# Kernel tuning notes

Measured on AMD Instinct MI355X. Metric: run time of the kernel, lower is better.

Reference implementation:

```python
import jax, jax.numpy as jnp
from jax import lax
import numpy as np

B, T, FEAT = 32, 256, 640
H, P = 2048, 640  # lstm_hidden_units, lstm_projection
FORGET_BIAS = 1.0  # TF v1 LSTMCell default


def setup_inputs() -> dict:
    key = jax.random.key(0)
    ks = jax.random.split(key, 6)
    s = 0.02  # small init so tanh/sigmoid stay well-conditioned
    return {
        "x": jax.random.normal(ks[0], (B, T, FEAT), dtype=jnp.float32),
        "W0": jax.random.normal(ks[1], (FEAT + P, 4 * H), dtype=jnp.float32) * s,
        "b0": jnp.zeros((4 * H,), dtype=jnp.float32),
        "P0": jax.random.normal(ks[2], (H, P), dtype=jnp.float32) * s,
        "W1": jax.random.normal(ks[3], (P + P, 4 * H), dtype=jnp.float32) * s,
        "b1": jnp.zeros((4 * H,), dtype=jnp.float32),
        "P1": jax.random.normal(ks[4], (H, P), dtype=jnp.float32) * s,
    }


def _lstmp_layer(x, W, b, proj):
    # x: [B, T, D]; TF v1 LSTMCell with num_proj, gate order (i, j, f, o)
    batch = x.shape[0]
    c0 = jnp.zeros((batch, H), dtype=x.dtype)
    m0 = jnp.zeros((batch, proj.shape[1]), dtype=x.dtype)

    def step(carry, xt):
        c, m = carry
        z = jnp.concatenate([xt, m], axis=-1) @ W + b  # [B, 4H]
        i, j, f, o = jnp.split(z, 4, axis=-1)
        c_new = jax.nn.sigmoid(f + FORGET_BIAS) * c + jax.nn.sigmoid(i) * jnp.tanh(j)
        m_new = (jax.nn.sigmoid(o) * jnp.tanh(c_new)) @ proj  # [B, P]
        return (c_new, m_new), m_new

    xT = jnp.swapaxes(x, 0, 1)  # [T, B, D]
    _, ys = lax.scan(step, (c0, m0), xT)
    return jnp.swapaxes(ys, 0, 1)  # [B, T, P]


def reference(x, W0, b0, P0, W1, b1, P1):
    h = _lstmp_layer(x, W0, b0, P0)
    h = _lstmp_layer(h, W1, b1, P1)
    return h
```

## Files before the change

### kernel.cpp

```cpp
#include <hip/hip_runtime.h>
#include <math.h>

typedef __attribute__((ext_vector_type(8))) short s16x8;
typedef __attribute__((ext_vector_type(8))) _Float16 f16x8;
typedef __attribute__((ext_vector_type(16))) float f32x16;
typedef unsigned long long u64;
typedef unsigned short u16;

#define NBLK 256
#define NTHR 512

constexpr int HSZ2 = 32 * 2048;

__device__ __forceinline__ float sigm(float v) { return 1.0f / (1.0f + expf(-v)); }

__device__ __forceinline__ unsigned short bf16_rne(float x) {
    unsigned u = __float_as_uint(x);
    return (unsigned short)((u + 0x7FFFu + ((u >> 16) & 1u)) >> 16);
}
__device__ __forceinline__ void split2(float x, unsigned short& hi, unsigned short& lo) {
    unsigned u = __float_as_uint(x);
    hi = (unsigned short)(u >> 16);
    float hf = __uint_as_float(u & 0xFFFF0000u);
    lo = bf16_rne(x - hf);
}
__device__ __forceinline__ void split8(const float* f, s16x8& h, s16x8& l) {
    #pragma unroll
    for (int i = 0; i < 8; ++i) {
        unsigned short hh, ll;
        split2(f[i], hh, ll);
        h[i] = (short)hh; l[i] = (short)ll;
    }
}

__device__ __forceinline__ void ast64(u16* p, u64 v) {
    __hip_atomic_store((u64*)p, v, __ATOMIC_RELAXED, __HIP_MEMORY_SCOPE_AGENT);
}

__device__ __forceinline__ void pollall(const unsigned* arr, unsigned e) {
    if (threadIdx.x < 64) {
        const int i0 = (int)threadIdx.x * 4;
        for (;;) {
            bool ok = (__hip_atomic_load(arr + i0 + 0, __ATOMIC_RELAXED, __HIP_MEMORY_SCOPE_AGENT) >= e) &&
                      (__hip_atomic_load(arr + i0 + 1, __ATOMIC_RELAXED, __HIP_MEMORY_SCOPE_AGENT) >= e) &&
                      (__hip_atomic_load(arr + i0 + 2, __ATOMIC_RELAXED, __HIP_MEMORY_SCOPE_AGENT) >= e) &&
                      (__hip_atomic_load(arr + i0 + 3, __ATOMIC_RELAXED, __HIP_MEMORY_SCOPE_AGENT) >= e);
            if (__all(ok)) break;
            __builtin_amdgcn_s_sleep(1);
        }
    }
    __syncthreads();
}

__global__ void transpose_split(const float* __restrict__ in,
                                u16* __restrict__ outHi, u16* __restrict__ outLo,
                                int R, int C) {
    __shared__ float tile[32][33];
    const int c0 = blockIdx.x * 32, r0 = blockIdx.y * 32;
    const int tid = threadIdx.x;
    {
        int r = tid >> 3, q = (tid & 7) * 4;
        float4 v = *(const float4*)(in + (size_t)(r0 + r) * C + c0 + q);
        tile[q + 0][r] = v.x; tile[q + 1][r] = v.y;
        tile[q + 2][r] = v.z; tile[q + 3][r] = v.w;
    }
    __syncthreads();
    {
        int c = tid >> 3, q = (tid & 7) * 4;
        ushort4 h, l;
        unsigned short hh, ll;
        split2(tile[c][q + 0], hh, ll); h.x = hh; l.x = ll;
        split2(tile[c][q + 1], hh, ll); h.y = hh; l.y = ll;
        split2(tile[c][q + 2], hh, ll); h.z = hh; l.z = ll;
        split2(tile[c][q + 3], hh, ll); h.w = hh; l.w = ll;
        size_t o = (size_t)(c0 + c) * R + r0 + q;
        *(ushort4*)(outHi + o) = h;
        *(ushort4*)(outLo + o) = l;
    }
}

__global__ void transpose_f16(const float* __restrict__ in, u16* __restrict__ outp,
                              int R, int C) {
    __shared__ float tile[32][33];
    const int c0 = blockIdx.x * 32, r0 = blockIdx.y * 32;
    const int tid = threadIdx.x;
    {
        int r = tid >> 3, q = (tid & 7) * 4;
        float4 v = *(const float4*)(in + (size_t)(r0 + r) * C + c0 + q);
        tile[q + 0][r] = v.x; tile[q + 1][r] = v.y;
        tile[q + 2][r] = v.z; tile[q + 3][r] = v.w;
    }
    __syncthreads();
    {
        int c = tid >> 3, q = (tid & 7) * 4;
        ushort4 o;
        o.x = __builtin_bit_cast(u16, (_Float16)tile[c][q + 0]);
        o.y = __builtin_bit_cast(u16, (_Float16)tile[c][q + 1]);
        o.z = __builtin_bit_cast(u16, (_Float16)tile[c][q + 2]);
        o.w = __builtin_bit_cast(u16, (_Float16)tile[c][q + 3]);
        *(ushort4*)(outp + (size_t)(c0 + c) * R + r0 + q) = o;
    }
}

__global__ void xcast(const float* __restrict__ in, u16* __restrict__ outp, int n4) {
    int i = blockIdx.x * blockDim.x + threadIdx.x;
    if (i < n4) {
        float4 v = ((const float4*)in)[i];
        ushort4 o;
        o.x = __builtin_bit_cast(u16, (_Float16)v.x);
        o.y = __builtin_bit_cast(u16, (_Float16)v.y);
        o.z = __builtin_bit_cast(u16, (_Float16)v.z);
        o.w = __builtin_bit_cast(u16, (_Float16)v.w);
        ((ushort4*)outp)[i] = o;
    }
}

__global__ void __launch_bounds__(256) qgemm(const float* __restrict__ P,
    const u16* __restrict__ WH, const u16* __restrict__ WL,
    u16* __restrict__ Qt, int rowOff) {
    const int tid = threadIdx.x;
    const int wid = tid >> 6, lane = tid & 63;
    const int n = lane & 31, kg = lane >> 5;
    const int tile = blockIdx.x * 4 + wid;
    const int ct = tile & 255, kt = tile >> 8;
    const int col = ct * 32 + n;
    const int krow = kt * 32 + n;

    f32x16 acc;
    #pragma unroll
    for (int r = 0; r < 16; ++r) acc[r] = 0.f;

    const float* ap = P + (size_t)krow * 640 + kg * 8;
    const u16* bhp = WH + (size_t)col * 1280 + rowOff + kg * 8;
    const u16* blp = WL + (size_t)col * 1280 + rowOff + kg * 8;
    #pragma unroll 4
    for (int ks = 0; ks < 40; ++ks) {
        float4 v0 = *(const float4*)(ap + ks * 16);
        float4 v1 = *(const float4*)(ap + ks * 16 + 4);
        float f[8] = {v0.x, v0.y, v0.z, v0.w, v1.x, v1.y, v1.z, v1.w};
        s16x8 ah, al;
        split8(f, ah, al);
        s16x8 bh = *(const s16x8*)(bhp + ks * 16);
        s16x8 bl = *(const s16x8*)(blp + ks * 16);
        acc = __builtin_amdgcn_mfma_f32_32x32x16_bf16(ah, bh, acc, 0, 0, 0);
        acc = __builtin_amdgcn_mfma_f32_32x32x16_bf16(ah, bl, acc, 0, 0, 0);
        acc = __builtin_amdgcn_mfma_f32_32x32x16_bf16(al, bh, acc, 0, 0, 0);
    }
    u16* qrow = Qt + (size_t)col * 2048 + kt * 32 + 4 * kg;
    #pragma unroll
    for (int q = 0; q < 4; ++q) {
        ushort4 o;
        o.x = __builtin_bit_cast(u16, (_Float16)acc[4 * q + 0]);
        o.y = __builtin_bit_cast(u16, (_Float16)acc[4 * q + 1]);
        o.z = __builtin_bit_cast(u16, (_Float16)acc[4 * q + 2]);
        o.w = __builtin_bit_cast(u16, (_Float16)acc[4 * q + 3]);
        *(ushort4*)(qrow + 8 * q) = o;
    }
}

__global__ void __launch_bounds__(NTHR, 1) lstm_pipe(
    const u16* __restrict__ xh,
    const float* __restrict__ bias0, const float* __restrict__ bias1,
    const u16* __restrict__ Wxt0,
    const u16* __restrict__ Qt0, const u16* __restrict__ Qt01, const u16* __restrict__ Qt1,
    const u16* __restrict__ Pt1,
    u16* __restrict__ hb0, u16* __restrict__ hb1,
    float* out, unsigned* arr) {
    __shared__ float part0[8][64][20];
    __shared__ float part1[8][64][20];
    __shared__ u16 hst0[32][8];
    __shared__ u16 hst1[32][8];

    const int tid = threadIdx.x, bid = blockIdx.x;
    const int wid = tid >> 6, lane = tid & 63;
    const int n = lane & 31, kg = lane >> 5;

    const int colmap = (n >> 3) * 2048 + bid * 8 + (n & 7);
    const size_t wx640 = (size_t)colmap * 640 + wid * 80 + kg * 8;
    const size_t qOff  = (size_t)colmap * 2048 + wid * 256 + kg * 8;
    const size_t aXh   = (size_t)n * (256 * 640) + wid * 80 + kg * 8;
    const size_t hROff = (size_t)n * 2048 + wid * 256 + kg * 8;

    const int rn = tid >> 4, rm0 = (tid & 15) * 2;

    const bool isC0 = tid < 256;
    const int cl = tid & 255;
    const int ch = cl >> 5, cb = cl & 31;
    float bv[4];
    #pragma unroll
    for (int gx = 0; gx < 4; ++gx)
        bv[gx] = (isC0 ? bias0 : bias1)[gx * 2048 + bid * 8 + ch];
    const int crg = (cb & 3) + 4 * (cb >> 3);
    const int clp = 32 * ((cb >> 2) & 1);

    uint4 q0r[16], q01r[16], q1r[16];
    #pragma unroll
    for (int ks = 0; ks < 16; ++ks) {
        q0r[ks]  = *(const uint4*)(Qt0  + qOff + ks * 16);
        q01r[ks] = *(const uint4*)(Qt01 + qOff + ks * 16);
        q1r[ks]  = *(const uint4*)(Qt1  + qOff + ks * 16);
    }
    #pragma unroll
    for (int ks = 0; ks < 16; ++ks) {
        asm volatile("" : "+v"(q0r[ks].x),  "+v"(q0r[ks].y),  "+v"(q0r[ks].z),  "+v"(q0r[ks].w));
        asm volatile("" : "+v"(q01r[ks].x), "+v"(q01r[ks].y), "+v"(q01r[ks].z), "+v"(q01r[ks].w));
        asm volatile("" : "+v"(q1r[ks].x),  "+v"(q1r[ks].y),  "+v"(q1r[ks].z),  "+v"(q1r[ks].w));
    }

    float creg = 0.f;

    auto xp0 = [&](int t) -> f32x16 {
        f32x16 a;
        #pragma unroll
        for (int r = 0; r < 16; ++r) a[r] = 0.f;
        const u16* xb = xh + aXh + (size_t)t * 640;
        const u16* wb = Wxt0 + wx640;
        #pragma unroll
        for (int ks = 0; ks < 5; ++ks)
            a = __builtin_amdgcn_mfma_f32_32x32x16_f16(*(const f16x8*)(xb + ks * 16),
                                                       *(const f16x8*)(wb + ks * 16), a, 0, 0, 0);
        return a;
    };
    auto stash = [&](float (*prt)[64][20], const f32x16& v) {
        #pragma unroll
        for (int r = 0; r < 4; ++r) {
            float4 w;
            w.x = v[4 * r + 0]; w.y = v[4 * r + 1];
            w.z = v[4 * r + 2]; w.w = v[4 * r + 3];
            *(float4*)&prt[wid][lane][4 * r] = w;
        }
    };

    f32x16 zacc0 = xp0(0);

    for (int g = 0; g <= 256; ++g) {
        if (g > 0) pollall(arr, (unsigned)g);
        const int s = g - 1;
        const bool doL0 = (g <= 255);
        const bool doL1 = (s >= 0);

        f32x16 acc0, acc1;
        if (doL0) acc0 = zacc0;
        if (doL1) {
            #pragma unroll
            for (int r = 0; r < 16; ++r) acc1[r] = 0.f;
        }
        if (g >= 1) {
            const u16* h0c = hb0 + (size_t)(g - 1) * HSZ2 + hROff;
            if (doL0) {
                #pragma unroll
                for (int ks = 0; ks < 16; ++ks) {
                    f16x8 a = *(const f16x8*)(h0c + ks * 16);
                    acc0 = __builtin_amdgcn_mfma_f32_32x32x16_f16(a, __builtin_bit_cast(f16x8, q0r[ks]),  acc0, 0, 0, 0);
                    acc1 = __builtin_amdgcn_mfma_f32_32x32x16_f16(a, __builtin_bit_cast(f16x8, q01r[ks]), acc1, 0, 0, 0);
                }
            } else {
                #pragma unroll
                for (int ks = 0; ks < 16; ++ks)
                    acc1 = __builtin_amdgcn_mfma_f32_32x32x16_f16(*(const f16x8*)(h0c + ks * 16),
                                                                  __builtin_bit_cast(f16x8, q01r[ks]), acc1, 0, 0, 0);
            }
        }
        if (s >= 1) {
            const u16* h1c = hb1 + (size_t)(s - 1) * HSZ2 + hROff;
            #pragma unroll
            for (int ks = 0; ks < 16; ++ks)
                acc1 = __builtin_amdgcn_mfma_f32_32x32x16_f16(*(const f16x8*)(h1c + ks * 16),
                                                              __builtin_bit_cast(f16x8, q1r[ks]), acc1, 0, 0, 0);
        }

        if (doL0) stash(part0, acc0);
        if (doL1) stash(part1, acc1);
        __syncthreads();
        if ((isC0 && doL0) || (!isC0 && doL1)) {
            float (*prt)[64][20] = isC0 ? part0 : part1;
            float z[4];
            #pragma unroll
            for (int gx = 0; gx < 4; ++gx) {
                const int lp = (gx * 8 + ch) + clp;
                float ssum = 0.f;
                #pragma unroll
                for (int w = 0; w < 8; ++w) ssum += prt[w][lp][crg];
                z[gx] = ssum + bv[gx];
            }
            float cn = sigm(z[2] + 1.0f) * creg + sigm(z[0]) * tanhf(z[1]);
            creg = cn;
            u16 hv = __builtin_bit_cast(u16, (_Float16)(sigm(z[3]) * tanhf(cn)));
            if (isC0) hst0[cb][ch] = hv;
            else      hst1[cb][ch] = hv;
        }
        __syncthreads();

        if (doL0 && wid == 0) {
            int b = tid >> 1, hf = tid & 1;
            u64 v = *(const u64*)&hst0[b][hf * 4];
            ast64(hb0 + (size_t)g * HSZ2 + (size_t)b * 2048 + bid * 8 + hf * 4, v);
        }
        if (doL1 && wid == 1) {
            int l = tid - 64;
            int b = l >> 1, hf = l & 1;
            u64 v = *(const u64*)&hst1[b][hf * 4];
            ast64(hb1 + (size_t)s * HSZ2 + (size_t)b * 2048 + bid * 8 + hf * 4, v);
        }
        __syncthreads();
        if (tid == 0)
            __hip_atomic_store(arr + bid, (unsigned)(g + 1), __ATOMIC_RELAXED, __HIP_MEMORY_SCOPE_AGENT);

        if (g < 255) zacc0 = xp0(g + 1);
    }

    pollall(arr, 257u);
    const int mb = bid >> 3;
    const int t0 = (bid * 32) & 255;
    const size_t aOff = (size_t)(t0 + n) * HSZ2 + (size_t)mb * 2048 + wid * 256 + kg * 8;
    for (int ct = 0; ct < 20; ++ct) {
        f32x16 pacc;
        #pragma unroll
        for (int r = 0; r < 16; ++r) pacc[r] = 0.f;
        const u16* ap = hb1 + aOff;
        const u16* bp = Pt1 + (size_t)(ct * 32 + n) * 2048 + wid * 256 + kg * 8;
        #pragma unroll
        for (int ks = 0; ks < 16; ++ks)
            pacc = __builtin_amdgcn_mfma_f32_32x32x16_f16(*(const f16x8*)(ap + ks * 16),
                                                          *(const f16x8*)(bp + ks * 16), pacc, 0, 0, 0);
        __syncthreads();
        stash(part0, pacc);
        __syncthreads();
        #pragma unroll
        for (int j = 0; j < 2; ++j) {
            int m = rm0 + j;
            int lp = rn + 32 * ((m >> 2) & 1);
            int rg = (m & 3) + 4 * (m >> 3);
            float ssum = 0.f;
            #pragma unroll
            for (int w = 0; w < 8; ++w) ssum += part0[w][lp][rg];
            out[(size_t)(bid * 32 + m) * 640 + ct * 32 + rn] = ssum;
        }
    }
}

__device__ __forceinline__ void grid_bar_slow(unsigned int* bar, unsigned int& epoch) {
    __syncthreads();
    epoch++;
    if (threadIdx.x == 0) {
        __threadfence();
        atomicAdd(bar, 1u);
        const unsigned int target = epoch * NBLK;
        while (__hip_atomic_load(bar, __ATOMIC_RELAXED, __HIP_MEMORY_SCOPE_AGENT) < target)
            __builtin_amdgcn_s_sleep(1);
        __threadfence();
    }
    __syncthreads();
}

__global__ void __launch_bounds__(NTHR, 1) lstm_fb(
    const float* __restrict__ x,
    const float* __restrict__ W0, const float* __restrict__ b0, const float* __restrict__ Pr0,
    const float* __restrict__ W1, const float* __restrict__ b1, const float* __restrict__ Pr1,
    float* out, float* ws) {
    const int tid = threadIdx.x;
    const int bid = blockIdx.x;
    unsigned int* bar = (unsigned int*)ws;
    float* mbuf0 = ws + 1024;
    float* mbuf1 = mbuf0 + 32 * 640;
    float* hws = mbuf1 + 32 * 640;
    __shared__ float zbuf[32 * 33];
    __shared__ float pred[512];
    unsigned int epoch = 0;
    const int c_idx = tid & 31;
    const int bg = tid >> 5;
    const int b0r = bg * 2;
    const int col = (c_idx >> 3) * 2048 + bid * 8 + (c_idx & 7);
    const int ch = tid >> 5;
    const int cb = tid & 31;
    const int p_s = (bid * 640) / NBLK;
    const int p_e = ((bid + 1) * 640) / NBLK;
    const int np = p_e - p_s;
    const int kq_n = (np == 2) ? 8 : 4;
    const int klen = 2048 / kq_n;
    const int pg = tid >> 5;
    const bool pact = pg < np * kq_n;
    const int pj = pact ? (pg % np) : 0;
    const int kq = pact ? (pg / np) : 0;
    for (int layer = 0; layer < 2; ++layer) {
        const float* W = layer ? W1 : W0;
        const float* bbv = layer ? b1 : b0;
        const float* Pr = layer ? Pr1 : Pr0;
        const float* inb = layer ? (const float*)out : x;
        for (int i = bid * NTHR + tid; i < 32 * 640; i += NBLK * NTHR) mbuf0[i] = 0.0f;
        float creg = 0.0f;
        grid_bar_slow(bar, epoch);
        const float bias = bbv[col];
        for (int t = 0; t < 256; ++t) {
            float* mcur = (t & 1) ? mbuf1 : mbuf0;
            float* mnxt = (t & 1) ? mbuf0 : mbuf1;
            const float* in0 = inb + (size_t)(b0r * 256 + t) * 640;
            const float* in1 = in0 + (size_t)256 * 640;
            const float* wp = W + col;
            float a0 = 0.f, a1 = 0.f;
            #pragma unroll 4
            for (int k = 0; k < 640; k += 4) {
                float4 u0 = *(const float4*)(in0 + k);
                float4 u1 = *(const float4*)(in1 + k);
                float w0 = wp[(size_t)(k + 0) * 8192], w1 = wp[(size_t)(k + 1) * 8192];
                float w2 = wp[(size_t)(k + 2) * 8192], w3 = wp[(size_t)(k + 3) * 8192];
                a0 += w0 * u0.x + w1 * u0.y + w2 * u0.z + w3 * u0.w;
                a1 += w0 * u1.x + w1 * u1.y + w2 * u1.z + w3 * u1.w;
            }
            const float* q0 = mcur + (size_t)b0r * 640;
            const float* q1 = q0 + 640;
            #pragma unroll 4
            for (int k = 0; k < 640; k += 4) {
                float4 u0 = *(const float4*)(q0 + k);
                float4 u1 = *(const float4*)(q1 + k);
                float w0 = wp[(size_t)(640 + k + 0) * 8192], w1 = wp[(size_t)(640 + k + 1) * 8192];
                float w2 = wp[(size_t)(640 + k + 2) * 8192], w3 = wp[(size_t)(640 + k + 3) * 8192];
                a0 += w0 * u0.x + w1 * u0.y + w2 * u0.z + w3 * u0.w;
                a1 += w0 * u1.x + w1 * u1.y + w2 * u1.z + w3 * u1.w;
            }
            zbuf[c_idx * 33 + b0r + 0] = a0 + bias;
            zbuf[c_idx * 33 + b0r + 1] = a1 + bias;
            __syncthreads();
            if (tid < 256) {
                float zi = zbuf[(0 * 8 + ch) * 33 + cb];
                float zj = zbuf[(1 * 8 + ch) * 33 + cb];
                float zf = zbuf[(2 * 8 + ch) * 33 + cb];
                float zo = zbuf[(3 * 8 + ch) * 33 + cb];
                float cn = sigm(zf + 1.0f) * creg + sigm(zi) * tanhf(zj);
                creg = cn;
                hws[(size_t)(bid * 8 + ch) * 32 + cb] = sigm(zo) * tanhf(cn);
            }
            grid_bar_slow(bar, epoch);
            if (pact) {
                const int p = p_s + pj;
                const float* pp = Pr + p;
                const int k0 = kq * klen;
                float s = 0.f;
                #pragma unroll 4
                for (int k = k0; k < k0 + klen; ++k) s += hws[(size_t)k * 32 + cb] * pp[(size_t)k * 640];
                pred[(pj * 32 + cb) * kq_n + kq] = s;
            }
            __syncthreads();
            if (tid < np * 32) {
                float s = 0.f;
                for (int q2 = 0; q2 < kq_n; ++q2) s += pred[tid * kq_n + q2];
                const int p = p_s + (tid >> 5);
                const int b = tid & 31;
                mnxt[(size_t)b * 640 + p] = s;
                out[((size_t)b * 256 + t) * 640 + p] = s;
            }
            grid_bar_slow(bar, epoch);
        }
    }
}

extern "C" void kernel_launch(void* const* d_in, const int* in_sizes, int n_in,
                              void* d_out, int out_size, void* d_ws, size_t ws_size,
                              hipStream_t stream) {
    const float* x   = (const float*)d_in[0];
    const float* W0  = (const float*)d_in[1];
    const float* b0  = (const float*)d_in[2];
    const float* P0  = (const float*)d_in[3];
    const float* W1  = (const float*)d_in[4];
    const float* b1  = (const float*)d_in[5];
    const float* P1  = (const float*)d_in[6];
    float* out = (float*)d_out;

    size_t off = 0;
    auto alloc = [&](size_t bytes) { size_t o = off; off += (bytes + 255) & ~(size_t)255; return o; };
    const size_t oBar  = alloc(32768);
    const size_t szW   = (size_t)8192 * 1280 * 2;
    const size_t szQ   = (size_t)8192 * 2048 * 2;
    const size_t szPt  = (size_t)640 * 2048 * 2;
    const size_t szWx  = (size_t)8192 * 640 * 2;
    const size_t oWH   = alloc(szW), oWL = alloc(szW);
    const size_t oQt0  = alloc(szQ), oQt01 = alloc(szQ), oQt1 = alloc(szQ);
    const size_t oPt1  = alloc(szPt);
    const size_t oWx0  = alloc(szWx);
    const size_t oXh   = alloc((size_t)32 * 256 * 640 * 2);
    const size_t oH0   = alloc((size_t)256 * HSZ2 * 2);
    const size_t oH1   = alloc((size_t)256 * HSZ2 * 2);
    const size_t need  = off;

    hipMemsetAsync(d_ws, 0, 32768, stream);

    if (ws_size < need) {
        float* ws = (float*)d_ws;
        void* args[] = {(void*)&x, (void*)&W0, (void*)&b0, (void*)&P0,
                        (void*)&W1, (void*)&b1, (void*)&P1, (void*)&out, (void*)&ws};
        hipError_t err = hipLaunchCooperativeKernel((const void*)lstm_fb,
                                                    dim3(NBLK), dim3(NTHR), args, 0, stream);
        if (err != hipSuccess)
            lstm_fb<<<dim3(NBLK), dim3(NTHR), 0, stream>>>(x, W0, b0, P0, W1, b1, P1, out, ws);
        return;
    }

    char* w = (char*)d_ws;
    u16 *WHp = (u16*)(w + oWH), *WLp = (u16*)(w + oWL);
    u16 *Qt0p = (u16*)(w + oQt0), *Qt01p = (u16*)(w + oQt01), *Qt1p = (u16*)(w + oQt1);
    u16 *Pt1p = (u16*)(w + oPt1);
    u16 *Wx0p = (u16*)(w + oWx0);
    u16 *xhp  = (u16*)(w + oXh);
    u16 *hb0p = (u16*)(w + oH0), *hb1p = (u16*)(w + oH1);
    unsigned* arrp = (unsigned*)(w + oBar);

    transpose_split<<<dim3(256, 40), 256, 0, stream>>>(W0, WHp, WLp, 1280, 8192);
    qgemm<<<dim3(4096), 256, 0, stream>>>(P0, WHp, WLp, Qt0p, 640);
    transpose_split<<<dim3(256, 40), 256, 0, stream>>>(W1, WHp, WLp, 1280, 8192);
    qgemm<<<dim3(4096), 256, 0, stream>>>(P0, WHp, WLp, Qt01p, 0);
    qgemm<<<dim3(4096), 256, 0, stream>>>(P1, WHp, WLp, Qt1p, 640);
    transpose_f16<<<dim3(20, 64), 256, 0, stream>>>(P1, Pt1p, 2048, 640);
    transpose_f16<<<dim3(256, 20), 256, 0, stream>>>(W0, Wx0p, 640, 8192);
    xcast<<<dim3(5120), 256, 0, stream>>>(x, xhp, 32 * 256 * 640 / 4);

    const float *b0c = b0, *b1c = b1;
    void* args[] = {(void*)&xhp, (void*)&b0c, (void*)&b1c,
                    (void*)&Wx0p,
                    (void*)&Qt0p, (void*)&Qt01p, (void*)&Qt1p, (void*)&Pt1p,
                    (void*)&hb0p, (void*)&hb1p,
                    (void*)&out, (void*)&arrp};
    hipError_t err = hipLaunchCooperativeKernel((const void*)lstm_pipe,
                                                dim3(NBLK), dim3(NTHR), args, 0, stream);
    if (err != hipSuccess)
        lstm_pipe<<<dim3(NBLK), dim3(NTHR), 0, stream>>>(
            xhp, b0c, b1c, Wx0p, Qt0p, Qt01p, Qt1p, Pt1p, hb0p, hb1p, out, arrp);
}
```

Before: 5.246 ms.

## Replace all-to-all flag polling with a single-master release barrier

Each step previously had every one of 256 blocks poll all 256 arrival flags. Now block 0 alone gathers the arrival flags and publishes one release counter, and the other blocks spin on that single word with one thread. The hidden-state stores from both layers are merged into one wavefront, which drains its own stores with s_waitcnt before signalling, removing a __syncthreads. This cuts polling traffic on the shared counters, but every step now takes an extra hop through block 0, which adds latency.

```diff
diff --git a/kernel.cpp b/kernel.cpp
--- a/kernel.cpp
+++ b/kernel.cpp
@@ -37,17 +37,10 @@
     __hip_atomic_store((u64*)p, v, __ATOMIC_RELAXED, __HIP_MEMORY_SCOPE_AGENT);
 }
 
-__device__ __forceinline__ void pollall(const unsigned* arr, unsigned e) {
-    if (threadIdx.x < 64) {
-        const int i0 = (int)threadIdx.x * 4;
-        for (;;) {
-            bool ok = (__hip_atomic_load(arr + i0 + 0, __ATOMIC_RELAXED, __HIP_MEMORY_SCOPE_AGENT) >= e) &&
-                      (__hip_atomic_load(arr + i0 + 1, __ATOMIC_RELAXED, __HIP_MEMORY_SCOPE_AGENT) >= e) &&
-                      (__hip_atomic_load(arr + i0 + 2, __ATOMIC_RELAXED, __HIP_MEMORY_SCOPE_AGENT) >= e) &&
-                      (__hip_atomic_load(arr + i0 + 3, __ATOMIC_RELAXED, __HIP_MEMORY_SCOPE_AGENT) >= e);
-            if (__all(ok)) break;
+__device__ __forceinline__ void pollrel(const unsigned* rel, unsigned e) {
+    if (threadIdx.x == 0) {
+        while (__hip_atomic_load(rel, __ATOMIC_RELAXED, __HIP_MEMORY_SCOPE_AGENT) < e)
             __builtin_amdgcn_s_sleep(1);
-        }
     }
     __syncthreads();
 }
@@ -165,7 +158,7 @@
     const u16* __restrict__ Qt0, const u16* __restrict__ Qt01, const u16* __restrict__ Qt1,
     const u16* __restrict__ Pt1,
     u16* __restrict__ hb0, u16* __restrict__ hb1,
-    float* out, unsigned* arr) {
+    float* out, unsigned* arr, unsigned* rel) {
     __shared__ float part0[8][64][20];
     __shared__ float part1[8][64][20];
     __shared__ u16 hst0[32][8];
@@ -234,7 +227,7 @@
     f32x16 zacc0 = xp0(0);
 
     for (int g = 0; g <= 256; ++g) {
-        if (g > 0) pollall(arr, (unsigned)g);
+        if (g > 0) pollrel(rel, (unsigned)g);
         const int s = g - 1;
         const bool doL0 = (g <= 255);
         const bool doL1 = (s >= 0);
@@ -291,25 +284,37 @@
         }
         __syncthreads();
 
-        if (doL0 && wid == 0) {
-            int b = tid >> 1, hf = tid & 1;
-            u64 v = *(const u64*)&hst0[b][hf * 4];
-            ast64(hb0 + (size_t)g * HSZ2 + (size_t)b * 2048 + bid * 8 + hf * 4, v);
-        }
-        if (doL1 && wid == 1) {
-            int l = tid - 64;
-            int b = l >> 1, hf = l & 1;
-            u64 v = *(const u64*)&hst1[b][hf * 4];
-            ast64(hb1 + (size_t)s * HSZ2 + (size_t)b * 2048 + bid * 8 + hf * 4, v);
-        }
-        __syncthreads();
-        if (tid == 0)
-            __hip_atomic_store(arr + bid, (unsigned)(g + 1), __ATOMIC_RELAXED, __HIP_MEMORY_SCOPE_AGENT);
-
+        if (wid == 0) {
+            const int b = tid >> 1, hf = tid & 1;
+            if (doL0)
+                ast64(hb0 + (size_t)g * HSZ2 + (size_t)b * 2048 + bid * 8 + hf * 4,
+                      *(const u64*)&hst0[b][hf * 4]);
+            if (doL1)
+                ast64(hb1 + (size_t)s * HSZ2 + (size_t)b * 2048 + bid * 8 + hf * 4,
+                      *(const u64*)&hst1[b][hf * 4]);
+            asm volatile("s_waitcnt vmcnt(0)" ::: "memory");
+            if (tid == 0)
+                __hip_atomic_store(arr + bid, (unsigned)(g + 1),
+                                   __ATOMIC_RELAXED, __HIP_MEMORY_SCOPE_AGENT);
+            if (bid == 0) {
+                const unsigned e = (unsigned)(g + 1);
+                const int i0 = tid * 4;
+                for (;;) {
+                    bool ok = (__hip_atomic_load(arr + i0 + 0, __ATOMIC_RELAXED, __HIP_MEMORY_SCOPE_AGENT) >= e) &&
+                              (__hip_atomic_load(arr + i0 + 1, __ATOMIC_RELAXED, __HIP_MEMORY_SCOPE_AGENT) >= e) &&
+                              (__hip_atomic_load(arr + i0 + 2, __ATOMIC_RELAXED, __HIP_MEMORY_SCOPE_AGENT) >= e) &&
+                              (__hip_atomic_load(arr + i0 + 3, __ATOMIC_RELAXED, __HIP_MEMORY_SCOPE_AGENT) >= e);
+                    if (__all(ok)) break;
+                    __builtin_amdgcn_s_sleep(1);
+                }
+                if (tid == 0)
+                    __hip_atomic_store(rel, e, __ATOMIC_RELAXED, __HIP_MEMORY_SCOPE_AGENT);
+            }
+        }
         if (g < 255) zacc0 = xp0(g + 1);
     }
 
-    pollall(arr, 257u);
+    pollrel(rel, 257u);
     const int mb = bid >> 3;
     const int t0 = (bid * 32) & 255;
     const size_t aOff = (size_t)(t0 + n) * HSZ2 + (size_t)mb * 2048 + wid * 256 + kg * 8;
@@ -503,6 +508,7 @@
     u16 *xhp  = (u16*)(w + oXh);
     u16 *hb0p = (u16*)(w + oH0), *hb1p = (u16*)(w + oH1);
     unsigned* arrp = (unsigned*)(w + oBar);
+    unsigned* relp = (unsigned*)(w + oBar + 2048);
 
     transpose_split<<<dim3(256, 40), 256, 0, stream>>>(W0, WHp, WLp, 1280, 8192);
     qgemm<<<dim3(4096), 256, 0, stream>>>(P0, WHp, WLp, Qt0p, 640);
@@ -518,10 +524,10 @@
                     (void*)&Wx0p,
                     (void*)&Qt0p, (void*)&Qt01p, (void*)&Qt1p, (void*)&Pt1p,
                     (void*)&hb0p, (void*)&hb1p,
-                    (void*)&out, (void*)&arrp};
+                    (void*)&out, (void*)&arrp, (void*)&relp};
     hipError_t err = hipLaunchCooperativeKernel((const void*)lstm_pipe,
                                                 dim3(NBLK), dim3(NTHR), args, 0, stream);
     if (err != hipSuccess)
         lstm_pipe<<<dim3(NBLK), dim3(NTHR), 0, stream>>>(
-            xhp, b0c, b1c, Wx0p, Qt0p, Qt01p, Qt1p, Pt1p, hb0p, hb1p, out, arrp);
-}
+            xhp, b0c, b1c, Wx0p, Qt0p, Qt01p, Qt1p, Pt1p, hb0p, hb1p, out, arrp, relp);
+}
```

Measured after the change: 5.671 ms. 1.08x slower.
